# Kernel optimization log

Hardware: AMD Instinct MI355X
Metric: run time of the kernel (lower is better)

The kernel has to match this reference:

```python
import jax, jax.numpy as jnp
import numpy as np

B, C, H, W = 8, 256, 32, 32
N_HEADS, N_GROUPS = 8, 4
HC = C // N_HEADS      # head channels = 32
GC = C // N_GROUPS     # group channels = 64
OFFSET_RANGE_FACTOR = 4.0


def dwconv3x3(x, w, b):
    # depthwise 3x3, stride 1, pad 1; x (B,Cc,H,W), w (Cc,1,3,3)
    y = jax.lax.conv_general_dilated(x, w, (1, 1), ((1, 1), (1, 1)),
                                     dimension_numbers=('NCHW', 'OIHW', 'NCHW'),
                                     feature_group_count=x.shape[1])
    return y + b[None, :, None, None]


def grid_sample_bilinear(img, pos_yx):
    # torch F.grid_sample, mode=bilinear, align_corners=True, padding_mode=zeros
    # img (BG,Cc,Hi,Wi); pos_yx (BG,Hs,Ws,2) in [-1,1], (y,x) order
    BG, Cc, Hi, Wi = img.shape
    Hs, Ws = pos_yx.shape[1], pos_yx.shape[2]
    y = (pos_yx[..., 0] + 1.0) * 0.5 * (Hi - 1)
    x = (pos_yx[..., 1] + 1.0) * 0.5 * (Wi - 1)
    y0 = jnp.floor(y); x0 = jnp.floor(x)
    yw = y - y0; xw = x - x0
    y0i = y0.astype(jnp.int32); x0i = x0.astype(jnp.int32)
    imgf = img.reshape(BG, Cc, Hi * Wi)

    def gather(yi, xi, wgt):
        valid = ((yi >= 0) & (yi < Hi) & (xi >= 0) & (xi < Wi)).astype(img.dtype)
        idx = jnp.clip(yi, 0, Hi - 1) * Wi + jnp.clip(xi, 0, Wi - 1)
        idx = jnp.broadcast_to(idx.reshape(BG, 1, Hs * Ws), (BG, Cc, Hs * Ws))
        vals = jnp.take_along_axis(imgf, idx, axis=2)
        return vals * (wgt * valid).reshape(BG, 1, Hs * Ws)

    out = (gather(y0i,     x0i,     (1 - yw) * (1 - xw))
         + gather(y0i,     x0i + 1, (1 - yw) * xw)
         + gather(y0i + 1, x0i,     yw * (1 - xw))
         + gather(y0i + 1, x0i + 1, yw * xw))
    return out.reshape(BG, Cc, Hs, Ws)


def setup_inputs() -> dict:
    key = jax.random.key(0)
    ks = jax.random.split(key, 16)
    s = 0.02
    return {
        'x': jax.random.normal(ks[0], (B, C, H, W), jnp.float32),
        'Wq': jax.random.normal(ks[1], (C, C), jnp.float32) * s,
        'bq': jax.random.normal(ks[2], (C,), jnp.float32) * s,
        'Wk': jax.random.normal(ks[3], (C, C), jnp.float32) * s,
        'bk': jax.random.normal(ks[4], (C,), jnp.float32) * s,
        'Wv': jax.random.normal(ks[5], (C, C), jnp.float32) * s,
        'bv': jax.random.normal(ks[6], (C,), jnp.float32) * s,
        'Wo': jax.random.normal(ks[7], (C, C), jnp.float32) * s,
        'bo': jax.random.normal(ks[8], (C,), jnp.float32) * s,
        'off_dw_w': jax.random.normal(ks[9], (GC, 1, 3, 3), jnp.float32) * s,
        'off_dw_b': jax.random.normal(ks[10], (GC,), jnp.float32) * s,
        'off_ln_g': jnp.ones((GC,), jnp.float32),
        'off_ln_b': jnp.zeros((GC,), jnp.float32),
        'off_pw_w': jax.random.normal(ks[11], (2, GC), jnp.float32) * s,
        'rpe_dw_w': jax.random.normal(ks[12], (C, 1, 3, 3), jnp.float32) * s,
        'rpe_dw_b': jax.random.normal(ks[13], (C,), jnp.float32) * s,
    }


def reference(x, Wq, bq, Wk, bk, Wv, bv, Wo, bo,
              off_dw_w, off_dw_b, off_ln_g, off_ln_b, off_pw_w,
              rpe_dw_w, rpe_dw_b):
    scale = HC ** -0.5
    # q projection (1x1 conv)
    q = jnp.einsum('oc,bchw->bohw', Wq, x) + bq[None, :, None, None]
    # offset prediction per group
    q_off = q.reshape(B * N_GROUPS, GC, H, W)
    o = dwconv3x3(q_off, off_dw_w, off_dw_b)
    mu = o.mean(axis=1, keepdims=True)
    var = ((o - mu) ** 2).mean(axis=1, keepdims=True)
    o = (o - mu) / jnp.sqrt(var + 1e-5) * off_ln_g[None, :, None, None] + off_ln_b[None, :, None, None]
    o = jax.nn.gelu(o, approximate=False)
    offset = jnp.einsum('oc,bchw->bohw', off_pw_w, o)  # (BG,2,Hk,Wk)
    Hk, Wk_ = offset.shape[2], offset.shape[3]
    n = Hk * Wk_
    offset_range = jnp.array([1.0 / (Hk - 1.0), 1.0 / (Wk_ - 1.0)], x.dtype).reshape(1, 2, 1, 1)
    offset = jnp.tanh(offset) * offset_range * OFFSET_RANGE_FACTOR
    offset = offset.transpose(0, 2, 3, 1)  # (BG,Hk,Wk,2) (y,x)
    ry = (jnp.linspace(0.5, Hk - 0.5, Hk, dtype=x.dtype) / (Hk - 1.0)) * 2.0 - 1.0
    rx = (jnp.linspace(0.5, Wk_ - 0.5, Wk_, dtype=x.dtype) / (Wk_ - 1.0)) * 2.0 - 1.0
    ref = jnp.stack(jnp.meshgrid(ry, rx, indexing='ij'), axis=-1)[None]  # (1,Hk,Wk,2)
    pos = offset + ref  # offset_range_factor >= 0: no clamp
    # irregular bilinear gather
    x_sampled = grid_sample_bilinear(x.reshape(B * N_GROUPS, GC, H, W), pos)
    x_sampled = x_sampled.reshape(B, C, n)
    # k/v projections on sampled points
    qf = q.reshape(B * N_HEADS, HC, H * W)
    k = (jnp.einsum('oc,bcn->bon', Wk, x_sampled) + bk[None, :, None]).reshape(B * N_HEADS, HC, n)
    v = (jnp.einsum('oc,bcn->bon', Wv, x_sampled) + bv[None, :, None]).reshape(B * N_HEADS, HC, n)
    attn = jnp.einsum('bcm,bcn->bmn', qf, k) * scale
    # dwc_pe residual positional encoding
    lepe = dwconv3x3(qf.reshape(B, C, H, W), rpe_dw_w, rpe_dw_b).reshape(B * N_HEADS, HC, H * W)
    attn = jax.nn.softmax(attn, axis=2)
    out = jnp.einsum('bmn,bcn->bcm', attn, v) + lepe
    out = out.reshape(B, C, H, W)
    y = jnp.einsum('oc,bchw->bohw', Wo, out) + bo[None, :, None, None]
    return y
```

## Files before the change

kernel.cpp:

```cpp
#include <hip/hip_runtime.h>
#include <math.h>


#define NPOS 1024

typedef float f32x4   __attribute__((ext_vector_type(4)));
typedef short bf16x8  __attribute__((ext_vector_type(8)));
typedef short short4v __attribute__((ext_vector_type(4)));
typedef unsigned uint4v __attribute__((ext_vector_type(4)));

__device__ __forceinline__ short f2bf(float f) {
    unsigned u = __float_as_uint(f);
    unsigned r = (u + 0x7FFFu + ((u >> 16) & 1u)) >> 16;
    return (short)r;
}
__device__ __forceinline__ float bf2f(short s) {
    return __uint_as_float(((unsigned)(unsigned short)s) << 16);
}
__device__ __forceinline__ unsigned cvtpk(float a, float b) {
    unsigned r;
    asm("v_cvt_pk_bf16_f32 %0, %1, %2" : "=v"(r) : "v"(a), "v"(b));
    return r;
}

__device__ __forceinline__ bf16x8 ldfrag(const short* base, int row, int KE,
                                         int s0, int s1, int swz) {
    const short* r = base + row * KE;
    short4v lo = *(const short4v*)(r + ((s0 ^ swz) << 2));
    short4v hi = *(const short4v*)(r + ((s1 ^ swz) << 2));
    bf16x8 f = {lo[0], lo[1], lo[2], lo[3], hi[0], hi[1], hi[2], hi[3]};
    return f;
}

__device__ __forceinline__ bf16x8 gfrag(const short* __restrict__ r, int g) {
    short4v lo = *(const short4v*)(r + 4 * g);
    short4v hi = *(const short4v*)(r + 16 + 4 * g);
    bf16x8 f = {lo[0], lo[1], lo[2], lo[3], hi[0], hi[1], hi[2], hi[3]};
    return f;
}

__device__ __forceinline__ void stpair(short* base, int row, int KE, int h, int swz,
                                       bf16x8 v8) {
    short4v lo = {v8[0], v8[1], v8[2], v8[3]};
    short4v hi = {v8[4], v8[5], v8[6], v8[7]};
    *(short4v*)(base + row * KE + (((2 * h) ^ swz) << 2)) = lo;
    *(short4v*)(base + row * KE + (((2 * h + 1) ^ swz) << 2)) = hi;
}
__device__ __forceinline__ void st1(short* base, int row, int KE, int h, int swz,
                                    short4v v4) {
    *(short4v*)(base + row * KE + ((h ^ swz) << 2)) = v4;
}

__global__ void cvt_w(const float* __restrict__ Wq, const float* __restrict__ Wk,
                      const float* __restrict__ Wv, const float* __restrict__ Wo,
                      short* __restrict__ Wb)
{
    int gid = blockIdx.x * 256 + threadIdx.x;
    const float* src = (gid < 65536) ? Wq : (gid < 131072) ? Wk
                     : (gid < 196608) ? Wv : Wo;
    Wb[gid] = f2bf(src[gid & 65535]);
}

__global__ __launch_bounds__(256) void transpose_x(const float* __restrict__ x,
                                                   short* __restrict__ xT)
{
    __shared__ float tile[64][69];
    const int p0 = blockIdx.x * 64, c0 = blockIdx.y * 64, b = blockIdx.z;
    const int t = threadIdx.x;
    #pragma unroll
    for (int i = 0; i < 4; ++i) {
        int id = t + i * 256;
        int row = id >> 4, q = id & 15;
        float4 v = *(const float4*)(x + ((long)(b * 256 + c0 + row)) * NPOS + p0 + q * 4);
        tile[row][q * 4 + 0] = v.x; tile[row][q * 4 + 1] = v.y;
        tile[row][q * 4 + 2] = v.z; tile[row][q * 4 + 3] = v.w;
    }
    __syncthreads();
    #pragma unroll
    for (int i = 0; i < 2; ++i) {
        int id = t + i * 256;
        int p = id >> 3, cg = id & 7;
        bf16x8 o;
        #pragma unroll
        for (int j = 0; j < 8; ++j) o[j] = f2bf(tile[cg * 8 + j][p]);
        *(bf16x8*)(xT + ((long)(b * 1024 + p0 + p)) * 256 + c0 + cg * 8) = o;
    }
}

template<int MODE>
__global__ __launch_bounds__(256) void gemm_mfma(
    const short* __restrict__ A, const short* __restrict__ Bt,
    const float* __restrict__ bias,
    float* __restrict__ outF, short* __restrict__ outT)
{
    __shared__ short As[2][64 * 64];
    __shared__ short Bs[2][64 * 64];
    const int t = threadIdx.x;
    const int n0 = blockIdx.x * 64, m0 = blockIdx.y * 64;
    const int b = blockIdx.z;
    const int lane = t & 63, w = t >> 6;
    const int wm = w >> 1, wn = w & 1;
    const int l15 = lane & 15, g = lane >> 4;
    const int srow = t >> 3, sp = t & 7;
    f32x4 z = {0.f, 0.f, 0.f, 0.f};
    f32x4 acc[2][2];
    acc[0][0] = z; acc[0][1] = z; acc[1][0] = z; acc[1][1] = z;

    bf16x8 ar[2], br[2];
    #pragma unroll
    for (int i = 0; i < 2; ++i) {
        int row = srow + i * 32;
        ar[i] = *(const bf16x8*)(A + (long)(m0 + row) * 256 + sp * 8);
        br[i] = *(const bf16x8*)(Bt + ((long)b * 1024 + n0 + row) * 256 + sp * 8);
        stpair(As[0], row, 64, sp, row & 15, ar[i]);
        stpair(Bs[0], row, 64, sp, row & 15, br[i]);
    }
    __syncthreads();

    for (int kt = 0; kt < 4; ++kt) {
        const int cur = kt & 1;
        if (kt < 3) {
            const int k0 = (kt + 1) * 64;
            #pragma unroll
            for (int i = 0; i < 2; ++i) {
                int row = srow + i * 32;
                ar[i] = *(const bf16x8*)(A + (long)(m0 + row) * 256 + k0 + sp * 8);
                br[i] = *(const bf16x8*)(Bt + ((long)b * 1024 + n0 + row) * 256 + k0 + sp * 8);
            }
        }
        #pragma unroll
        for (int kk = 0; kk < 2; ++kk) {
            bf16x8 af[2], bfr[2];
            #pragma unroll
            for (int mi = 0; mi < 2; ++mi) {
                int row = wm * 32 + mi * 16 + l15;
                af[mi] = ldfrag(As[cur], row, 64, kk * 8 + g, kk * 8 + 4 + g, row & 15);
            }
            #pragma unroll
            for (int ni = 0; ni < 2; ++ni) {
                int row = wn * 32 + ni * 16 + l15;
                bfr[ni] = ldfrag(Bs[cur], row, 64, kk * 8 + g, kk * 8 + 4 + g, row & 15);
            }
            __builtin_amdgcn_s_setprio(1);
            #pragma unroll
            for (int mi = 0; mi < 2; ++mi)
                #pragma unroll
                for (int ni = 0; ni < 2; ++ni)
                    acc[mi][ni] = __builtin_amdgcn_mfma_f32_16x16x32_bf16(
                        af[mi], bfr[ni], acc[mi][ni], 0, 0, 0);
            __builtin_amdgcn_s_setprio(0);
        }
        if (kt < 3) {
            #pragma unroll
            for (int i = 0; i < 2; ++i) {
                int row = srow + i * 32;
                stpair(As[cur ^ 1], row, 64, sp, row & 15, ar[i]);
                stpair(Bs[cur ^ 1], row, 64, sp, row & 15, br[i]);
            }
        }
        __syncthreads();
    }
    #pragma unroll
    for (int mi = 0; mi < 2; ++mi) {
        const int mbase = m0 + wm * 32 + mi * 16 + g * 4;
        float bv[4];
        #pragma unroll
        for (int j = 0; j < 4; ++j) bv[j] = bias[mbase + j];
        #pragma unroll
        for (int ni = 0; ni < 2; ++ni) {
            const int n = n0 + wn * 32 + ni * 16 + l15;
            f32x4 r = acc[mi][ni];
            #pragma unroll
            for (int j = 0; j < 4; ++j) r[j] += bv[j];
            #pragma unroll
            for (int j = 0; j < 4; ++j)
                outF[((long)b * 256 + mbase + j) * NPOS + n] = r[j];
            if constexpr (MODE == 0) {
                const float sc = 0.25503486f;
                short4v p = {f2bf(r[0] * sc), f2bf(r[1] * sc),
                             f2bf(r[2] * sc), f2bf(r[3] * sc)};
                int bh = b * 8 + (mbase >> 5);
                *(short4v*)(outT + ((long)bh * 1024 + n) * 32 + (mbase & 31)) = p;
            }
        }
    }
}

__global__ __launch_bounds__(256) void gemm_kv(
    const short* __restrict__ Ak, const short* __restrict__ Av,
    const short* __restrict__ Bt,
    const float* __restrict__ bk, const float* __restrict__ bv,
    short* __restrict__ kT, short* __restrict__ vN)
{
    __shared__ short Ks[2][64 * 64];
    __shared__ short Vs[2][64 * 64];
    __shared__ short Bs[2][64 * 64];
    const int t = threadIdx.x;
    const int n0 = blockIdx.x * 64, m0 = blockIdx.y * 64;
    const int b = blockIdx.z;
    const int lane = t & 63, w = t >> 6;
    const int wm = w >> 1, wn = w & 1;
    const int l15 = lane & 15, g = lane >> 4;
    const int srow = t >> 3, sp = t & 7;
    f32x4 z = {0.f, 0.f, 0.f, 0.f};
    f32x4 acck[2][2], accv[2][2];
    acck[0][0] = z; acck[0][1] = z; acck[1][0] = z; acck[1][1] = z;
    accv[0][0] = z; accv[0][1] = z; accv[1][0] = z; accv[1][1] = z;

    bf16x8 a1[2], a2[2], bb[2];
    #pragma unroll
    for (int i = 0; i < 2; ++i) {
        int row = srow + i * 32;
        a1[i] = *(const bf16x8*)(Ak + (long)(m0 + row) * 256 + sp * 8);
        a2[i] = *(const bf16x8*)(Av + (long)(m0 + row) * 256 + sp * 8);
        bb[i] = *(const bf16x8*)(Bt + ((long)b * 1024 + n0 + row) * 256 + sp * 8);
        stpair(Ks[0], row, 64, sp, row & 15, a1[i]);
        stpair(Vs[0], row, 64, sp, row & 15, a2[i]);
        stpair(Bs[0], row, 64, sp, row & 15, bb[i]);
    }
    __syncthreads();

    for (int kt = 0; kt < 4; ++kt) {
        const int cur = kt & 1;
        if (kt < 3) {
            const int k0 = (kt + 1) * 64;
            #pragma unroll
            for (int i = 0; i < 2; ++i) {
                int row = srow + i * 32;
                a1[i] = *(const bf16x8*)(Ak + (long)(m0 + row) * 256 + k0 + sp * 8);
                a2[i] = *(const bf16x8*)(Av + (long)(m0 + row) * 256 + k0 + sp * 8);
                bb[i] = *(const bf16x8*)(Bt + ((long)b * 1024 + n0 + row) * 256 + k0 + sp * 8);
            }
        }
        #pragma unroll
        for (int kk = 0; kk < 2; ++kk) {
            bf16x8 afk[2], afv[2], bfr[2];
            #pragma unroll
            for (int mi = 0; mi < 2; ++mi) {
                int row = wm * 32 + mi * 16 + l15;
                afk[mi] = ldfrag(Ks[cur], row, 64, kk * 8 + g, kk * 8 + 4 + g, row & 15);
                afv[mi] = ldfrag(Vs[cur], row, 64, kk * 8 + g, kk * 8 + 4 + g, row & 15);
            }
            #pragma unroll
            for (int ni = 0; ni < 2; ++ni) {
                int row = wn * 32 + ni * 16 + l15;
                bfr[ni] = ldfrag(Bs[cur], row, 64, kk * 8 + g, kk * 8 + 4 + g, row & 15);
            }
            __builtin_amdgcn_s_setprio(1);
            #pragma unroll
            for (int mi = 0; mi < 2; ++mi)
                #pragma unroll
                for (int ni = 0; ni < 2; ++ni) {
                    acck[mi][ni] = __builtin_amdgcn_mfma_f32_16x16x32_bf16(
                        afk[mi], bfr[ni], acck[mi][ni], 0, 0, 0);
                    accv[mi][ni] = __builtin_amdgcn_mfma_f32_16x16x32_bf16(
                        afv[mi], bfr[ni], accv[mi][ni], 0, 0, 0);
                }
            __builtin_amdgcn_s_setprio(0);
        }
        if (kt < 3) {
            #pragma unroll
            for (int i = 0; i < 2; ++i) {
                int row = srow + i * 32;
                stpair(Ks[cur ^ 1], row, 64, sp, row & 15, a1[i]);
                stpair(Vs[cur ^ 1], row, 64, sp, row & 15, a2[i]);
                stpair(Bs[cur ^ 1], row, 64, sp, row & 15, bb[i]);
            }
        }
        __syncthreads();
    }
    #pragma unroll
    for (int mi = 0; mi < 2; ++mi) {
        const int mbase = m0 + wm * 32 + mi * 16 + g * 4;
        float bk4[4], bv4[4];
        #pragma unroll
        for (int j = 0; j < 4; ++j) { bk4[j] = bk[mbase + j]; bv4[j] = bv[mbase + j]; }
        #pragma unroll
        for (int ni = 0; ni < 2; ++ni) {
            const int n = n0 + wn * 32 + ni * 16 + l15;
            f32x4 rk = acck[mi][ni], rv = accv[mi][ni];
            short4v pk = {f2bf(rk[0] + bk4[0]), f2bf(rk[1] + bk4[1]),
                          f2bf(rk[2] + bk4[2]), f2bf(rk[3] + bk4[3])};
            int bh = b * 8 + (mbase >> 5);
            *(short4v*)(kT + ((long)bh * 1024 + n) * 32 + (mbase & 31)) = pk;
            #pragma unroll
            for (int j = 0; j < 4; ++j)
                vN[((long)b * 256 + mbase + j) * NPOS + n] = f2bf(rv[j] + bv4[j]);
        }
    }
}

__global__ __launch_bounds__(256) void offset_kernel(const float* __restrict__ q,
    const float* __restrict__ dww, const float* __restrict__ dwb,
    const float* __restrict__ lng, const float* __restrict__ lnb,
    const float* __restrict__ pww, float* __restrict__ pos)
{
    __shared__ float q3[64][3][33];
    __shared__ float wS[576];
    __shared__ float bS[64], gS[64], lbS[64], pS[128];
    const int t = threadIdx.x;
    const int y = blockIdx.x, bg = blockIdx.y;
    const float* qb = q + (long)bg * 64 * NPOS;
    for (int i = t; i < 576; i += 256) wS[i] = dww[i];
    if (t < 64) { bS[t] = dwb[t]; gS[t] = lng[t]; lbS[t] = lnb[t]; }
    else if (t >= 128 && t < 256) pS[t - 128] = pww[t - 128];
    #pragma unroll
    for (int i = 0; i < 6; ++i) {
        int id = t + i * 256;
        int c = id / 24, rx = id - c * 24;
        int r = rx >> 3, q4 = (rx & 7) * 4;
        int yy = y + r - 1;
        float4 v = make_float4(0.f, 0.f, 0.f, 0.f);
        if (yy >= 0 && yy < 32)
            v = *(const float4*)(qb + (long)c * NPOS + yy * 32 + q4);
        q3[c][r][q4 + 0] = v.x; q3[c][r][q4 + 1] = v.y;
        q3[c][r][q4 + 2] = v.z; q3[c][r][q4 + 3] = v.w;
    }
    __syncthreads();
    const int p = t >> 3, cg = t & 7;
    float oc[8];
    float s = 0.f, s2 = 0.f;
    #pragma unroll
    for (int j = 0; j < 8; ++j) {
        int c = cg * 8 + j;
        float acc = bS[c];
        #pragma unroll
        for (int dy = 0; dy < 3; ++dy)
            #pragma unroll
            for (int dx = 0; dx < 3; ++dx) {
                int xx = p + dx - 1;
                if (xx >= 0 && xx < 32)
                    acc += wS[c * 9 + dy * 3 + dx] * q3[c][dy][xx];
            }
        oc[j] = acc;
        s += acc; s2 += acc * acc;
    }
    s  += __shfl_xor(s, 1);  s  += __shfl_xor(s, 2);  s  += __shfl_xor(s, 4);
    s2 += __shfl_xor(s2, 1); s2 += __shfl_xor(s2, 2); s2 += __shfl_xor(s2, 4);
    float mu = s * 0.015625f;
    float var = s2 * 0.015625f - mu * mu;
    float rstd = rsqrtf(var + 1e-5f);
    float a0 = 0.f, a1 = 0.f;
    #pragma unroll
    for (int j = 0; j < 8; ++j) {
        int c = cg * 8 + j;
        float on = (oc[j] - mu) * rstd * gS[c] + lbS[c];
        float ge = 0.5f * on * (1.f + erff(on * 0.70710678118654752f));
        a0 += pS[c] * ge;
        a1 += pS[64 + c] * ge;
    }
    a0 += __shfl_xor(a0, 1); a0 += __shfl_xor(a0, 2); a0 += __shfl_xor(a0, 4);
    a1 += __shfl_xor(a1, 1); a1 += __shfl_xor(a1, 2); a1 += __shfl_xor(a1, 4);
    if (cg == 0) {
        const float rng = 4.f / 31.f;
        float offy = tanhf(a0) * rng;
        float offx = tanhf(a1) * rng;
        float ry = ((y + 0.5f) / 31.f) * 2.f - 1.f;
        float rx = ((p + 0.5f) / 31.f) * 2.f - 1.f;
        int pp = y * 32 + p;
        pos[(long)bg * 2048 + pp * 2 + 0] = offy + ry;
        pos[(long)bg * 2048 + pp * 2 + 1] = offx + rx;
    }
}

__global__ __launch_bounds__(256) void sample_kernel(const short* __restrict__ xT,
    const float* __restrict__ pos, short* __restrict__ xsT)
{
    const int wid = blockIdx.x * 4 + (threadIdx.x >> 6);
    const int l = threadIdx.x & 63;
    const int p = wid & 1023, bg = wid >> 10;
    const float py = pos[(long)bg * 2048 + p * 2 + 0];
    const float px = pos[(long)bg * 2048 + p * 2 + 1];
    const float fy = (py + 1.f) * 15.5f;
    const float fx = (px + 1.f) * 15.5f;
    const float y0f = floorf(fy), x0f = floorf(fx);
    const int y0 = (int)y0f, x0 = (int)x0f;
    const float yw = fy - y0f, xw = fx - x0f;
    const short* base = xT + ((long)(bg >> 2) * 1024) * 256 + (bg & 3) * 64 + l;
    float acc = 0.f;
    { int yi = y0,     xi = x0;     float wg = (1.f - yw) * (1.f - xw);
      if (yi >= 0 && yi < 32 && xi >= 0 && xi < 32)
          acc += wg * bf2f(base[(long)(yi * 32 + xi) * 256]); }
    { int yi = y0,     xi = x0 + 1; float wg = (1.f - yw) * xw;
      if (yi >= 0 && yi < 32 && xi >= 0 && xi < 32)
          acc += wg * bf2f(base[(long)(yi * 32 + xi) * 256]); }
    { int yi = y0 + 1, xi = x0;     float wg = yw * (1.f - xw);
      if (yi >= 0 && yi < 32 && xi >= 0 && xi < 32)
          acc += wg * bf2f(base[(long)(yi * 32 + xi) * 256]); }
    { int yi = y0 + 1, xi = x0 + 1; float wg = yw * xw;
      if (yi >= 0 && yi < 32 && xi >= 0 && xi < 32)
          acc += wg * bf2f(base[(long)(yi * 32 + xi) * 256]); }
    xsT[((long)(bg >> 2) * 1024 + p) * 256 + (bg & 3) * 64 + l] = f2bf(acc);
}

__global__ __launch_bounds__(512) void attn_mfma(
    const short* __restrict__ qT, const short* __restrict__ kT,
    const short* __restrict__ vN, const float* __restrict__ qf,
    const float* __restrict__ rdw, const float* __restrict__ rdb,
    short* __restrict__ aoutT)
{
    __shared__ short kS[2][64 * 32];
    __shared__ short vS[2][32 * 64];
    __shared__ float oT[128 * 33];
    __shared__ short qr[6][32][33];
    __shared__ float wR[288], bR[32];
    const int t = threadIdx.x;
    const int bid = blockIdx.x;
    const int bh = (bid & 7) * 8 + ((bid >> 3) & 7);
    const int mt = bid >> 6;
    const int m0 = mt * 128;
    const int lane = t & 63, w = t >> 6;
    const int l15 = lane & 15, g = lane >> 4;
    const long base32 = (long)bh * 32768;
    const int c0 = (bh & 7) * 32;
    const int krow_ = t >> 3, kh = t & 7;
    const int vc = t >> 4, vh = t & 15;
    f32x4 z = {0.f, 0.f, 0.f, 0.f};

    {
        const int y0 = (m0 >> 5) - 1;
        #pragma unroll
        for (int i = 0; i < 3; ++i) {
            int id = t + i * 512;
            int xq = id & 7, cc = (id >> 3) & 31, r = id >> 8;
            int yy = y0 + r;
            float4 v = make_float4(0.f, 0.f, 0.f, 0.f);
            if (yy >= 0 && yy < 32)
                v = *(const float4*)(qf + base32 + (long)cc * NPOS + yy * 32 + xq * 4);
            qr[r][cc][xq * 4 + 0] = f2bf(v.x); qr[r][cc][xq * 4 + 1] = f2bf(v.y);
            qr[r][cc][xq * 4 + 2] = f2bf(v.z); qr[r][cc][xq * 4 + 3] = f2bf(v.w);
        }
        if (t < 32) bR[t] = rdb[c0 + t];
        for (int i = t; i < 288; i += 512) wR[i] = rdw[c0 * 9 + i];
    }

    const int qrow = w * 16 + l15;
    const bf16x8 qb = gfrag(qT + base32 + (long)(m0 + qrow) * 32, g);

    short4v kr1 = *(const short4v*)(kT + base32 + (long)krow_ * 32 + kh * 4);
    short4v vr1 = *(const short4v*)(vN + base32 + (long)vc * NPOS + vh * 4);
    st1(kS[0], krow_, 32, kh, (krow_ >> 1) & 7, kr1);
    st1(vS[0], vc, 64, vh, vc & 15, vr1);
    __syncthreads();

    f32x4 Lacc = z;
    f32x4 po[2]; po[0] = z; po[1] = z;

    for (int nt = 0; nt < 16; ++nt) {
        const int cur = nt & 1;
        if (nt < 15) {
            const int n0n = (nt + 1) * 64;
            kr1 = *(const short4v*)(kT + base32 + (long)(n0n + krow_) * 32 + kh * 4);
            vr1 = *(const short4v*)(vN + base32 + (long)vc * NPOS + n0n + vh * 4);
        }
        f32x4 s[4];
        #pragma unroll
        for (int j = 0; j < 4; ++j) {
            int krow = j * 16 + l15;
            bf16x8 ka = ldfrag(kS[cur], krow, 32, g, 4 + g, (krow >> 1) & 7);
            s[j] = __builtin_amdgcn_mfma_f32_16x16x32_bf16(ka, qb, z, 0, 0, 0);
        }
        #pragma unroll
        for (int j = 0; j < 4; ++j) {
            #pragma unroll
            for (int r = 0; r < 4; ++r) s[j][r] = exp2f(s[j][r]);
            Lacc += s[j];
        }
        bf16x8 pb[2];
        #pragma unroll
        for (int ks = 0; ks < 2; ++ks) {
            uint4v u;
            u[0] = cvtpk(s[2 * ks][0], s[2 * ks][1]);
            u[1] = cvtpk(s[2 * ks][2], s[2 * ks][3]);
            u[2] = cvtpk(s[2 * ks + 1][0], s[2 * ks + 1][1]);
            u[3] = cvtpk(s[2 * ks + 1][2], s[2 * ks + 1][3]);
            pb[ks] = __builtin_bit_cast(bf16x8, u);
        }
        #pragma unroll
        for (int cs = 0; cs < 2; ++cs) {
            int vrow = cs * 16 + l15;
            #pragma unroll
            for (int ks = 0; ks < 2; ++ks) {
                bf16x8 va = ldfrag(vS[cur], vrow, 64, ks * 8 + g, ks * 8 + 4 + g, vrow & 15);
                po[cs] = __builtin_amdgcn_mfma_f32_16x16x32_bf16(va, pb[ks], po[cs], 0, 0, 0);
            }
        }
        if (nt < 15) {
            st1(kS[cur ^ 1], krow_, 32, kh, (krow_ >> 1) & 7, kr1);
            st1(vS[cur ^ 1], vc, 64, vh, vc & 15, vr1);
        }
        __syncthreads();
    }
    float ls = Lacc[0] + Lacc[1] + Lacc[2] + Lacc[3];
    ls += __shfl_xor(ls, 16);
    ls += __shfl_xor(ls, 32);
    float inv = 1.f / ls;
    #pragma unroll
    for (int cs = 0; cs < 2; ++cs)
        #pragma unroll
        for (int r = 0; r < 4; ++r)
            oT[qrow * 33 + cs * 16 + g * 4 + r] = po[cs][r] * inv;
    __syncthreads();
    #pragma unroll
    for (int i = 0; i < 8; ++i) {
        int idx = t + i * 512;
        int c = idx & 31, m = idx >> 5;
        int ml = m >> 5, xx0 = m & 31;
        float acc = 0.f;
        #pragma unroll
        for (int dy = 0; dy < 3; ++dy)
            #pragma unroll
            for (int dx = 0; dx < 3; ++dx) {
                int xx = xx0 + dx - 1;
                if (xx >= 0 && xx < 32)
                    acc += wR[c * 9 + dy * 3 + dx] * bf2f(qr[ml + dy][c][xx]);
            }
        float v = oT[m * 33 + c] + acc + bR[c];
        aoutT[(((long)(bh >> 3)) * 1024 + m0 + m) * 256 + (bh & 7) * 32 + c] = f2bf(v);
    }
}

extern "C" void kernel_launch(void* const* d_in, const int* in_sizes, int n_in,
                              void* d_out, int out_size, void* d_ws, size_t ws_size,
                              hipStream_t stream)
{
    const float* x   = (const float*)d_in[0];
    const float* Wq  = (const float*)d_in[1];
    const float* bq  = (const float*)d_in[2];
    const float* Wk  = (const float*)d_in[3];
    const float* bk  = (const float*)d_in[4];
    const float* Wv  = (const float*)d_in[5];
    const float* bv  = (const float*)d_in[6];
    const float* Wo  = (const float*)d_in[7];
    const float* bo  = (const float*)d_in[8];
    const float* odw = (const float*)d_in[9];
    const float* odb = (const float*)d_in[10];
    const float* olg = (const float*)d_in[11];
    const float* olb = (const float*)d_in[12];
    const float* opw = (const float*)d_in[13];
    const float* rdw = (const float*)d_in[14];
    const float* rdb = (const float*)d_in[15];

    float* ws = (float*)d_ws;
    const size_t SZ = (size_t)2097152;
    float* qf  = ws;
    float* pos = ws + SZ;
    short* sb  = (short*)(ws + SZ + 65536);
    short* Wb  = sb;
    short* xT  = Wb + 262144;
    short* xsT = xT + SZ;
    short* qTb = xsT + SZ;
    short* kTb = qTb + SZ;
    short* vNb = kTb + SZ;
    float* y   = (float*)d_out;
    short* aoT = xsT;

    dim3 gg(16, 4, 8);
    cvt_w<<<1024, 256, 0, stream>>>(Wq, Wk, Wv, Wo, Wb);
    transpose_x<<<gg, 256, 0, stream>>>(x, xT);
    gemm_mfma<0><<<gg, 256, 0, stream>>>(Wb, xT, bq, qf, qTb);
    offset_kernel<<<dim3(32, 32), 256, 0, stream>>>(qf, odw, odb, olg, olb, opw, pos);
    sample_kernel<<<8192, 256, 0, stream>>>(xT, pos, xsT);
    gemm_kv<<<gg, 256, 0, stream>>>(Wb + 65536, Wb + 131072, xsT, bk, bv, kTb, vNb);
    attn_mfma<<<512, 512, 0, stream>>>(qTb, kTb, vNb, qf, rdw, rdb, aoT);
    gemm_mfma<3><<<gg, 256, 0, stream>>>(Wb + 196608, aoT, bo, y, nullptr);
}
```

Baseline: 86.02 us.

## Fuse weight conversion into transpose, fuse sampling into offset kernel, split attention KV range

The fp32-to-bf16 weight conversion now runs as an extra z-slice of the transpose launch, and bilinear sampling moves into the offset kernel, so the pos buffer and two launches go away. The attention kernel gives each group of four warps half of the key range, with its own double-buffered K/V tiles. Each warp handles two 16-row query fragments so K fragments are reused, and the two halves' partial outputs and row sums are merged through shared memory. This trims launch overhead and redundant global traffic, at the cost of more registers and shared memory in the attention kernel.

```diff
diff --git a/kernel.cpp b/kernel.cpp
--- a/kernel.cpp
+++ b/kernel.cpp
@@ -46,27 +46,27 @@
     *(short4v*)(base + row * KE + (((2 * h) ^ swz) << 2)) = lo;
     *(short4v*)(base + row * KE + (((2 * h + 1) ^ swz) << 2)) = hi;
 }
-__device__ __forceinline__ void st1(short* base, int row, int KE, int h, int swz,
-                                    short4v v4) {
-    *(short4v*)(base + row * KE + ((h ^ swz) << 2)) = v4;
-}
-
-__global__ void cvt_w(const float* __restrict__ Wq, const float* __restrict__ Wk,
-                      const float* __restrict__ Wv, const float* __restrict__ Wo,
-                      short* __restrict__ Wb)
+
+__global__ __launch_bounds__(256) void transpose_x(const float* __restrict__ x,
+    short* __restrict__ xT,
+    const float* __restrict__ Wq, const float* __restrict__ Wk,
+    const float* __restrict__ Wv, const float* __restrict__ Wo,
+    short* __restrict__ Wb)
 {
-    int gid = blockIdx.x * 256 + threadIdx.x;
-    const float* src = (gid < 65536) ? Wq : (gid < 131072) ? Wk
-                     : (gid < 196608) ? Wv : Wo;
-    Wb[gid] = f2bf(src[gid & 65535]);
-}
-
-__global__ __launch_bounds__(256) void transpose_x(const float* __restrict__ x,
-                                                   short* __restrict__ xT)
-{
+    const int t = threadIdx.x;
+    if (blockIdx.z == 8) {
+        int gid = (blockIdx.y * 16 + blockIdx.x) * 256 + t;
+        #pragma unroll
+        for (int i = 0; i < 16; ++i) {
+            int idx = gid + i * 16384;
+            const float* src = (idx < 65536) ? Wq : (idx < 131072) ? Wk
+                             : (idx < 196608) ? Wv : Wo;
+            Wb[idx] = f2bf(src[idx & 65535]);
+        }
+        return;
+    }
     __shared__ float tile[64][69];
     const int p0 = blockIdx.x * 64, c0 = blockIdx.y * 64, b = blockIdx.z;
-    const int t = threadIdx.x;
     #pragma unroll
     for (int i = 0; i < 4; ++i) {
         int id = t + i * 256;
@@ -290,10 +290,11 @@
     }
 }
 
-__global__ __launch_bounds__(256) void offset_kernel(const float* __restrict__ q,
+__global__ __launch_bounds__(256) void offset_sample(
+    const float* __restrict__ q, const short* __restrict__ xT,
     const float* __restrict__ dww, const float* __restrict__ dwb,
     const float* __restrict__ lng, const float* __restrict__ lnb,
-    const float* __restrict__ pww, float* __restrict__ pos)
+    const float* __restrict__ pww, short* __restrict__ xsT)
 {
     __shared__ float q3[64][3][33];
     __shared__ float wS[576];
@@ -351,70 +352,59 @@
     }
     a0 += __shfl_xor(a0, 1); a0 += __shfl_xor(a0, 2); a0 += __shfl_xor(a0, 4);
     a1 += __shfl_xor(a1, 1); a1 += __shfl_xor(a1, 2); a1 += __shfl_xor(a1, 4);
-    if (cg == 0) {
-        const float rng = 4.f / 31.f;
-        float offy = tanhf(a0) * rng;
-        float offx = tanhf(a1) * rng;
-        float ry = ((y + 0.5f) / 31.f) * 2.f - 1.f;
-        float rx = ((p + 0.5f) / 31.f) * 2.f - 1.f;
-        int pp = y * 32 + p;
-        pos[(long)bg * 2048 + pp * 2 + 0] = offy + ry;
-        pos[(long)bg * 2048 + pp * 2 + 1] = offx + rx;
-    }
-}
-
-__global__ __launch_bounds__(256) void sample_kernel(const short* __restrict__ xT,
-    const float* __restrict__ pos, short* __restrict__ xsT)
-{
-    const int wid = blockIdx.x * 4 + (threadIdx.x >> 6);
-    const int l = threadIdx.x & 63;
-    const int p = wid & 1023, bg = wid >> 10;
-    const float py = pos[(long)bg * 2048 + p * 2 + 0];
-    const float px = pos[(long)bg * 2048 + p * 2 + 1];
-    const float fy = (py + 1.f) * 15.5f;
-    const float fx = (px + 1.f) * 15.5f;
-    const float y0f = floorf(fy), x0f = floorf(fx);
-    const int y0 = (int)y0f, x0 = (int)x0f;
-    const float yw = fy - y0f, xw = fx - x0f;
-    const short* base = xT + ((long)(bg >> 2) * 1024) * 256 + (bg & 3) * 64 + l;
-    float acc = 0.f;
-    { int yi = y0,     xi = x0;     float wg = (1.f - yw) * (1.f - xw);
-      if (yi >= 0 && yi < 32 && xi >= 0 && xi < 32)
-          acc += wg * bf2f(base[(long)(yi * 32 + xi) * 256]); }
-    { int yi = y0,     xi = x0 + 1; float wg = (1.f - yw) * xw;
-      if (yi >= 0 && yi < 32 && xi >= 0 && xi < 32)
-          acc += wg * bf2f(base[(long)(yi * 32 + xi) * 256]); }
-    { int yi = y0 + 1, xi = x0;     float wg = yw * (1.f - xw);
-      if (yi >= 0 && yi < 32 && xi >= 0 && xi < 32)
-          acc += wg * bf2f(base[(long)(yi * 32 + xi) * 256]); }
-    { int yi = y0 + 1, xi = x0 + 1; float wg = yw * xw;
-      if (yi >= 0 && yi < 32 && xi >= 0 && xi < 32)
-          acc += wg * bf2f(base[(long)(yi * 32 + xi) * 256]); }
-    xsT[((long)(bg >> 2) * 1024 + p) * 256 + (bg & 3) * 64 + l] = f2bf(acc);
-}
-
-__global__ __launch_bounds__(512) void attn_mfma(
+    const float rng = 4.f / 31.f;
+    float py = tanhf(a0) * rng + ((y + 0.5f) / 31.f) * 2.f - 1.f;
+    float px = tanhf(a1) * rng + ((p + 0.5f) / 31.f) * 2.f - 1.f;
+    float fy = (py + 1.f) * 15.5f;
+    float fx = (px + 1.f) * 15.5f;
+    float y0f = floorf(fy), x0f = floorf(fx);
+    int y0 = (int)y0f, x0 = (int)x0f;
+    float yw = fy - y0f, xw = fx - x0f;
+    const short* base = xT + ((long)(bg >> 2) * 1024) * 256 + (bg & 3) * 64 + cg * 8;
+    float acc8[8] = {};
+    #pragma unroll
+    for (int cy = 0; cy < 2; ++cy)
+        #pragma unroll
+        for (int cx = 0; cx < 2; ++cx) {
+            int yi = y0 + cy, xi = x0 + cx;
+            float wg = (cy ? yw : 1.f - yw) * (cx ? xw : 1.f - xw);
+            if (yi >= 0 && yi < 32 && xi >= 0 && xi < 32) {
+                bf16x8 v8 = *(const bf16x8*)(base + (long)(yi * 32 + xi) * 256);
+                #pragma unroll
+                for (int j = 0; j < 8; ++j) acc8[j] += wg * bf2f(v8[j]);
+            }
+        }
+    bf16x8 o;
+    #pragma unroll
+    for (int j = 0; j < 8; ++j) o[j] = f2bf(acc8[j]);
+    *(bf16x8*)(xsT + ((long)(bg >> 2) * 1024 + y * 32 + p) * 256 + (bg & 3) * 64 + cg * 8) = o;
+}
+
+__global__ __launch_bounds__(512, 4) void attn_mfma(
     const short* __restrict__ qT, const short* __restrict__ kT,
     const short* __restrict__ vN, const float* __restrict__ qf,
     const float* __restrict__ rdw, const float* __restrict__ rdb,
     short* __restrict__ aoutT)
 {
-    __shared__ short kS[2][64 * 32];
-    __shared__ short vS[2][32 * 64];
+    __shared__ short kS[2][2][64 * 32];
+    __shared__ short vS[2][2][32 * 64];
     __shared__ float oT[128 * 33];
     __shared__ short qr[6][32][33];
-    __shared__ float wR[288], bR[32];
+    __shared__ float wR[288], bR[32], Lb[2][128];
     const int t = threadIdx.x;
     const int bid = blockIdx.x;
     const int bh = (bid & 7) * 8 + ((bid >> 3) & 7);
     const int mt = bid >> 6;
     const int m0 = mt * 128;
     const int lane = t & 63, w = t >> 6;
+    const int g2 = w >> 2, gw = w & 3;
     const int l15 = lane & 15, g = lane >> 4;
     const long base32 = (long)bh * 32768;
     const int c0 = (bh & 7) * 32;
-    const int krow_ = t >> 3, kh = t & 7;
-    const int vc = t >> 4, vh = t & 15;
+    const int tg = t & 255;
+    const int krow_ = tg >> 2, kh = tg & 3;
+    const int vc = tg >> 3, vh = tg & 7;
+    const int nbase = g2 * 512;
     f32x4 z = {0.f, 0.f, 0.f, 0.f};
 
     {
@@ -434,78 +424,113 @@
         for (int i = t; i < 288; i += 512) wR[i] = rdw[c0 * 9 + i];
     }
 
-    const int qrow = w * 16 + l15;
-    const bf16x8 qb = gfrag(qT + base32 + (long)(m0 + qrow) * 32, g);
-
-    short4v kr1 = *(const short4v*)(kT + base32 + (long)krow_ * 32 + kh * 4);
-    short4v vr1 = *(const short4v*)(vN + base32 + (long)vc * NPOS + vh * 4);
-    st1(kS[0], krow_, 32, kh, (krow_ >> 1) & 7, kr1);
-    st1(vS[0], vc, 64, vh, vc & 15, vr1);
-    __syncthreads();
-
-    f32x4 Lacc = z;
-    f32x4 po[2]; po[0] = z; po[1] = z;
-
-    for (int nt = 0; nt < 16; ++nt) {
-        const int cur = nt & 1;
-        if (nt < 15) {
-            const int n0n = (nt + 1) * 64;
-            kr1 = *(const short4v*)(kT + base32 + (long)(n0n + krow_) * 32 + kh * 4);
-            vr1 = *(const short4v*)(vN + base32 + (long)vc * NPOS + n0n + vh * 4);
-        }
-        f32x4 s[4];
+    int qrow[2]; bf16x8 qb[2];
+    #pragma unroll
+    for (int f = 0; f < 2; ++f) {
+        qrow[f] = gw * 32 + f * 16 + l15;
+        qb[f] = gfrag(qT + base32 + (long)(m0 + qrow[f]) * 32, g);
+    }
+
+    bf16x8 kr = *(const bf16x8*)(kT + base32 + (long)(nbase + krow_) * 32 + kh * 8);
+    bf16x8 vr = *(const bf16x8*)(vN + base32 + (long)vc * NPOS + nbase + vh * 8);
+    stpair(kS[g2][0], krow_, 32, kh, (krow_ >> 1) & 7, kr);
+    stpair(vS[g2][0], vc, 64, vh, vc & 15, vr);
+    __syncthreads();
+
+    f32x4 Lacc[2]; Lacc[0] = z; Lacc[1] = z;
+    f32x4 po[2][2];
+    po[0][0] = z; po[0][1] = z; po[1][0] = z; po[1][1] = z;
+
+    for (int it = 0; it < 8; ++it) {
+        const int cur = it & 1;
+        if (it < 7) {
+            const int n0n = nbase + (it + 1) * 64;
+            kr = *(const bf16x8*)(kT + base32 + (long)(n0n + krow_) * 32 + kh * 8);
+            vr = *(const bf16x8*)(vN + base32 + (long)vc * NPOS + n0n + vh * 8);
+        }
+        bf16x8 ka[4];
         #pragma unroll
         for (int j = 0; j < 4; ++j) {
-            int krow = j * 16 + l15;
-            bf16x8 ka = ldfrag(kS[cur], krow, 32, g, 4 + g, (krow >> 1) & 7);
-            s[j] = __builtin_amdgcn_mfma_f32_16x16x32_bf16(ka, qb, z, 0, 0, 0);
-        }
-        #pragma unroll
-        for (int j = 0; j < 4; ++j) {
-            #pragma unroll
-            for (int r = 0; r < 4; ++r) s[j][r] = exp2f(s[j][r]);
-            Lacc += s[j];
-        }
-        bf16x8 pb[2];
-        #pragma unroll
-        for (int ks = 0; ks < 2; ++ks) {
-            uint4v u;
-            u[0] = cvtpk(s[2 * ks][0], s[2 * ks][1]);
-            u[1] = cvtpk(s[2 * ks][2], s[2 * ks][3]);
-            u[2] = cvtpk(s[2 * ks + 1][0], s[2 * ks + 1][1]);
-            u[3] = cvtpk(s[2 * ks + 1][2], s[2 * ks + 1][3]);
-            pb[ks] = __builtin_bit_cast(bf16x8, u);
-        }
+            int kr2 = j * 16 + l15;
+            ka[j] = ldfrag(kS[g2][cur], kr2, 32, g, 4 + g, (kr2 >> 1) & 7);
+        }
+        f32x4 s[2][4];
+        #pragma unroll
+        for (int f = 0; f < 2; ++f)
+            #pragma unroll
+            for (int j = 0; j < 4; ++j)
+                s[f][j] = __builtin_amdgcn_mfma_f32_16x16x32_bf16(ka[j], qb[f], z, 0, 0, 0);
+        #pragma unroll
+        for (int f = 0; f < 2; ++f)
+            #pragma unroll
+            for (int j = 0; j < 4; ++j) {
+                #pragma unroll
+                for (int r = 0; r < 4; ++r) s[f][j][r] = exp2f(s[f][j][r]);
+                Lacc[f] += s[f][j];
+            }
+        bf16x8 pb[2][2];
+        #pragma unroll
+        for (int f = 0; f < 2; ++f)
+            #pragma unroll
+            for (int ks = 0; ks < 2; ++ks) {
+                uint4v u;
+                u[0] = cvtpk(s[f][2 * ks][0], s[f][2 * ks][1]);
+                u[1] = cvtpk(s[f][2 * ks][2], s[f][2 * ks][3]);
+                u[2] = cvtpk(s[f][2 * ks + 1][0], s[f][2 * ks + 1][1]);
+                u[3] = cvtpk(s[f][2 * ks + 1][2], s[f][2 * ks + 1][3]);
+                pb[f][ks] = __builtin_bit_cast(bf16x8, u);
+            }
         #pragma unroll
         for (int cs = 0; cs < 2; ++cs) {
             int vrow = cs * 16 + l15;
             #pragma unroll
             for (int ks = 0; ks < 2; ++ks) {
-                bf16x8 va = ldfrag(vS[cur], vrow, 64, ks * 8 + g, ks * 8 + 4 + g, vrow & 15);
-                po[cs] = __builtin_amdgcn_mfma_f32_16x16x32_bf16(va, pb[ks], po[cs], 0, 0, 0);
-            }
-        }
-        if (nt < 15) {
-            st1(kS[cur ^ 1], krow_, 32, kh, (krow_ >> 1) & 7, kr1);
-            st1(vS[cur ^ 1], vc, 64, vh, vc & 15, vr1);
+                bf16x8 va = ldfrag(vS[g2][cur], vrow, 64, ks * 8 + g, ks * 8 + 4 + g, vrow & 15);
+                #pragma unroll
+                for (int f = 0; f < 2; ++f)
+                    po[cs][f] = __builtin_amdgcn_mfma_f32_16x16x32_bf16(
+                        va, pb[f][ks], po[cs][f], 0, 0, 0);
+            }
+        }
+        if (it < 7) {
+            stpair(kS[g2][cur ^ 1], krow_, 32, kh, (krow_ >> 1) & 7, kr);
+            stpair(vS[g2][cur ^ 1], vc, 64, vh, vc & 15, vr);
         }
         __syncthreads();
     }
-    float ls = Lacc[0] + Lacc[1] + Lacc[2] + Lacc[3];
-    ls += __shfl_xor(ls, 16);
-    ls += __shfl_xor(ls, 32);
-    float inv = 1.f / ls;
-    #pragma unroll
-    for (int cs = 0; cs < 2; ++cs)
-        #pragma unroll
-        for (int r = 0; r < 4; ++r)
-            oT[qrow * 33 + cs * 16 + g * 4 + r] = po[cs][r] * inv;
+    #pragma unroll
+    for (int f = 0; f < 2; ++f) {
+        float ls = Lacc[f][0] + Lacc[f][1] + Lacc[f][2] + Lacc[f][3];
+        ls += __shfl_xor(ls, 16);
+        ls += __shfl_xor(ls, 32);
+        if (lane < 16) Lb[g2][gw * 32 + f * 16 + lane] = ls;
+    }
+    if (g2 == 0) {
+        #pragma unroll
+        for (int cs = 0; cs < 2; ++cs)
+            #pragma unroll
+            for (int f = 0; f < 2; ++f)
+                #pragma unroll
+                for (int r = 0; r < 4; ++r)
+                    oT[qrow[f] * 33 + cs * 16 + g * 4 + r] = po[cs][f][r];
+    }
+    __syncthreads();
+    if (g2 == 1) {
+        #pragma unroll
+        for (int cs = 0; cs < 2; ++cs)
+            #pragma unroll
+            for (int f = 0; f < 2; ++f)
+                #pragma unroll
+                for (int r = 0; r < 4; ++r)
+                    oT[qrow[f] * 33 + cs * 16 + g * 4 + r] += po[cs][f][r];
+    }
     __syncthreads();
     #pragma unroll
     for (int i = 0; i < 8; ++i) {
         int idx = t + i * 512;
         int c = idx & 31, m = idx >> 5;
         int ml = m >> 5, xx0 = m & 31;
+        float inv = 1.f / (Lb[0][m] + Lb[1][m]);
         float acc = 0.f;
         #pragma unroll
         for (int dy = 0; dy < 3; ++dy)
@@ -515,7 +540,7 @@
                 if (xx >= 0 && xx < 32)
                     acc += wR[c * 9 + dy * 3 + dx] * bf2f(qr[ml + dy][c][xx]);
             }
-        float v = oT[m * 33 + c] + acc + bR[c];
+        float v = oT[m * 33 + c] * inv + acc + bR[c];
         aoutT[(((long)(bh >> 3)) * 1024 + m0 + m) * 256 + (bh & 7) * 32 + c] = f2bf(v);
     }
 }
@@ -544,8 +569,7 @@
     float* ws = (float*)d_ws;
     const size_t SZ = (size_t)2097152;
     float* qf  = ws;
-    float* pos = ws + SZ;
-    short* sb  = (short*)(ws + SZ + 65536);
+    short* sb  = (short*)(ws + SZ);
     short* Wb  = sb;
     short* xT  = Wb + 262144;
     short* xsT = xT + SZ;
@@ -555,12 +579,10 @@
     float* y   = (float*)d_out;
     short* aoT = xsT;
 
-    dim3 gg(16, 4, 8);
-    cvt_w<<<1024, 256, 0, stream>>>(Wq, Wk, Wv, Wo, Wb);
-    transpose_x<<<gg, 256, 0, stream>>>(x, xT);
+    dim3 gg(16, 4, 8), gg9(16, 4, 9);
+    transpose_x<<<gg9, 256, 0, stream>>>(x, xT, Wq, Wk, Wv, Wo, Wb);
     gemm_mfma<0><<<gg, 256, 0, stream>>>(Wb, xT, bq, qf, qTb);
-    offset_kernel<<<dim3(32, 32), 256, 0, stream>>>(qf, odw, odb, olg, olb, opw, pos);
-    sample_kernel<<<8192, 256, 0, stream>>>(xT, pos, xsT);
+    offset_sample<<<dim3(32, 32), 256, 0, stream>>>(qf, xT, odw, odb, olg, olb, opw, xsT);
     gemm_kv<<<gg, 256, 0, stream>>>(Wb + 65536, Wb + 131072, xsT, bk, bv, kTb, vNb);
     attn_mfma<<<512, 512, 0, stream>>>(qTb, kTb, vNb, qf, rdw, rdb, aoT);
     gemm_mfma<3><<<gg, 256, 0, stream>>>(Wb + 196608, aoT, bo, y, nullptr);
```

Result: faster. 74.20 us (-13.7%).
